# Kernel tuning notes

Measured on AMD Instinct MI355X. Metric: run time of the kernel, lower is better.

Reference implementation:

```python
import jax, jax.numpy as jnp
import numpy as np

N, D, H = 1024, 256, 512


def _linear_init(key, fan_in, fan_out):
    kw, kb = jax.random.split(key)
    bound = 1.0 / np.sqrt(fan_in)
    w = jax.random.uniform(kw, (fan_in, fan_out), jnp.float32, -bound, bound)
    b = jax.random.uniform(kb, (fan_out,), jnp.float32, -bound, bound)
    return w, b


def setup_inputs() -> dict:
    key = jax.random.key(0)
    ks = jax.random.split(key, 8)
    domain_a = jax.random.normal(ks[0], (N, D), jnp.float32)
    domain_b = jax.random.normal(ks[1], (N, D), jnp.float32)
    mu_w0, mu_b0 = _linear_init(ks[2], D, H)
    mu_w1, mu_b1 = _linear_init(ks[3], H, H)
    mu_w2, mu_b2 = _linear_init(ks[4], H, D)
    lv_w0, lv_b0 = _linear_init(ks[5], D, H)
    lv_w1, lv_b1 = _linear_init(ks[6], H, H)
    lv_w2, lv_b2 = _linear_init(ks[7], H, D)
    return dict(domain_a=domain_a, domain_b=domain_b,
                mu_w0=mu_w0, mu_b0=mu_b0, mu_w1=mu_w1, mu_b1=mu_b1, mu_w2=mu_w2, mu_b2=mu_b2,
                lv_w0=lv_w0, lv_b0=lv_b0, lv_w1=lv_w1, lv_b1=lv_b1, lv_w2=lv_w2, lv_b2=lv_b2)


def _net(x, ws, bs, final_act):
    h = x
    for i in range(len(ws)):
        h = h @ ws[i] + bs[i]
        if i < len(ws) - 1:
            h = jax.nn.relu(h)
    return final_act(h)


def _l2norm(h):
    # L2NormEncoder == F.normalize(dim=-1), eps clamp like torch
    n = jnp.maximum(jnp.linalg.norm(h, axis=-1, keepdims=True), 1e-12)
    return h / n


def reference(domain_a, domain_b, mu_w0, mu_b0, mu_w1, mu_b1, mu_w2, mu_b2,
              lv_w0, lv_b0, lv_w1, lv_b1, lv_w2, lv_b2):
    mu_ws, mu_bs = [mu_w0, mu_w1, mu_w2], [mu_b0, mu_b1, mu_b2]
    lv_ws, lv_bs = [lv_w0, lv_w1, lv_w2], [lv_b0, lv_b1, lv_b2]

    # ---- embedding-model loss: prob-model params frozen (requires_grad=False) ----
    sg = jax.lax.stop_gradient
    mu = _net(domain_a, [sg(w) for w in mu_ws], [sg(b) for b in mu_bs], _l2norm)
    log_var = _net(domain_a, [sg(w) for w in lv_ws], [sg(b) for b in lv_bs], jnp.tanh)
    inv_var = jnp.exp(-log_var)                                  # [N, D]
    pos_probs = jnp.sum(-(domain_b - mu) ** 2 * inv_var - log_var, axis=-1)  # [N]
    # pairwise: [i, j, d] = b[j, d] - mu[i, d]; mean over j
    diff2_mean = jnp.mean((domain_b[None, :, :] - mu[:, None, :]) ** 2, axis=1)  # [N, D]
    neg_probs = jnp.sum(-diff2_mean * inv_var - log_var, axis=-1)  # [N]
    embed_model_loss = jnp.mean(pos_probs - neg_probs)

    # ---- prob-model loss: embeddings detached, params trainable ----
    a_d, b_d = sg(domain_a), sg(domain_b)
    mu2 = _net(a_d, mu_ws, mu_bs, _l2norm)
    lv2 = _net(a_d, lv_ws, lv_bs, jnp.tanh)
    prob_model_loss = jnp.mean(jnp.sum((b_d - mu2) ** 2 * jnp.exp(-lv2) + lv2, axis=-1))

    emb_coef, prob_coef = 1.0, 1.0
    loss = emb_coef * embed_model_loss + prob_coef * prob_model_loss
    return loss
```

## Files before the change

### kernel.cpp

```cpp
#include <hip/hip_runtime.h>
#include <hip/hip_fp16.h>

#define N_ROWS 1024
#define DIM 256
#define HID 512

typedef _Float16 half_t;
typedef __attribute__((ext_vector_type(8))) _Float16 half8v;
typedef __attribute__((ext_vector_type(16))) float f32x16;

#define WS_CH 2560
#define AS_CH 2560

struct Params {
    const float* a;
    const float* b;
    const float* w[6];
    const float* bias[6];
    unsigned* c1;
    unsigned* c2;
    unsigned* c3;
    unsigned* cs;
    float* acc;
    unsigned* done;
    float* part_s;
    float* part_s2;
    float* raw[2];
    half_t* h1[2];
    half_t* h2[2];
    float* out;
};

__device__ __forceinline__ void flag_add(unsigned* c) {
    asm volatile("s_waitcnt vmcnt(0)" ::: "memory");
    __syncthreads();
    if (threadIdx.x == 0)
        __hip_atomic_fetch_add(c, 1u, __ATOMIC_RELAXED, __HIP_MEMORY_SCOPE_AGENT);
}
__device__ __forceinline__ void flag_wait(unsigned* c, unsigned tgt) {
    if (threadIdx.x == 0) {
        while (__hip_atomic_load(c, __ATOMIC_RELAXED, __HIP_MEMORY_SCOPE_AGENT) < tgt)
            __builtin_amdgcn_s_sleep(1);
        asm volatile("" ::: "memory");
    }
    __syncthreads();
}

template <int K>
__device__ __forceinline__ void stage_W(const float* __restrict__ W, const int Nout,
                                        const int bn, half_t* __restrict__ Ws) {
    const int tid = threadIdx.x;
    const int wk0 = tid >> 4, wn0 = (tid & 15) * 4;
    #pragma unroll 2
    for (int c = 0; c < K / 32; ++c) {
        float4 v0 = *(const float4*)&W[(c * 32 + wk0) * Nout + bn + wn0];
        float4 v1 = *(const float4*)&W[(c * 32 + wk0 + 16) * Nout + bn + wn0];
        half_t* dst = Ws + c * WS_CH;
        #pragma unroll
        for (int s = 0; s < 2; ++s) {
            const int wk = wk0 + s * 16;
            float4 v = s ? v1 : v0;
            #pragma unroll
            for (int j = 0; j < 4; ++j) {
                const int row = wn0 + j;
                const int cidx = (((wk >> 3) ^ ((row >> 3) & 3)) * 8) + (wk & 7);
                float e = (j == 0) ? v.x : (j == 1) ? v.y : (j == 2) ? v.z : v.w;
                dst[row * 40 + cidx] = (half_t)e;
            }
        }
    }
}

template <int K, int AF32, int MODE>
__device__ __forceinline__ void gemm_phase(const void* __restrict__ Av,
                                           const float* __restrict__ bias,
                                           void* __restrict__ Cp,
                                           const int Nout, const int bm, const int bn,
                                           const half_t* __restrict__ Ws,
                                           half_t* __restrict__ As) {
    const int tid = threadIdx.x;
    const int wave = tid >> 6, lane = tid & 63;
    const int wr = (wave >> 1) * 32, wc = (wave & 1) * 32;
    const int lr = lane & 31, hi = lane >> 5;
    const int sr = tid >> 2, skb = tid & 3;
    const int adst = (skb ^ ((sr >> 3) & 3)) * 8;
    const int ra = wr + lr, rb = wc + lr;
    const int sa = (ra >> 3) & 3, sb = (rb >> 3) & 3;
    const int a0off = (hi ^ sa) * 8, a1off = ((hi + 2) ^ sa) * 8;
    const int b0off = (hi ^ sb) * 8, b1off = ((hi + 2) ^ sb) * 8;
    constexpr int NC = K >> 5;

    const float* Af = (const float*)Av;
    const half_t* Ah = (const half_t*)Av;

    f32x16 acc;
    #pragma unroll
    for (int i = 0; i < 16; ++i) acc[i] = 0.f;

    float4 r0a, r0b, r1a, r1b;
    #define LOAD_A(c, xa, xb)                                                   \
        do {                                                                    \
            if (AF32) {                                                         \
                xa = *(const float4*)&Af[(bm + sr) * K + (c) * 32 + skb * 8];   \
                xb = *(const float4*)&Af[(bm + sr) * K + (c) * 32 + skb * 8 + 4]; \
            } else {                                                            \
                xa = *(const float4*)&Ah[(bm + sr) * K + (c) * 32 + skb * 8];   \
            }                                                                   \
        } while (0)
    #define WRITE_A(buf, xa, xb)                                                \
        do {                                                                    \
            half_t* d = As + (buf) * AS_CH + sr * 40 + adst;                    \
            if (AF32) {                                                         \
                half8v h;                                                       \
                h[0] = (half_t)xa.x; h[1] = (half_t)xa.y;                       \
                h[2] = (half_t)xa.z; h[3] = (half_t)xa.w;                       \
                h[4] = (half_t)xb.x; h[5] = (half_t)xb.y;                       \
                h[6] = (half_t)xb.z; h[7] = (half_t)xb.w;                       \
                *(half8v*)d = h;                                                \
            } else {                                                            \
                *(float4*)d = xa;                                               \
            }                                                                   \
        } while (0)

    LOAD_A(0, r0a, r0b);
    LOAD_A(1, r1a, r1b);
    WRITE_A(0, r0a, r0b);
    if (NC > 2) LOAD_A(2, r0a, r0b);

    for (int c = 0; c < NC; ++c) {
        const int w = c + 1;
        if (w < NC) {
            if (w & 1) { WRITE_A(w % 3, r1a, r1b); }
            else       { WRITE_A(w % 3, r0a, r0b); }
        }
        const int fch = c + 3;
        if (fch < NC) {
            if (fch & 1) { LOAD_A(fch, r1a, r1b); }
            else         { LOAD_A(fch, r0a, r0b); }
        }
        __syncthreads();
        const half_t* ab = As + (c % 3) * AS_CH;
        const half_t* wb = Ws + c * WS_CH;
        half8v av0 = *(const half8v*)&ab[ra * 40 + a0off];
        half8v bv0 = *(const half8v*)&wb[rb * 40 + b0off];
        acc = __builtin_amdgcn_mfma_f32_32x32x16_f16(av0, bv0, acc, 0, 0, 0);
        half8v av1 = *(const half8v*)&ab[ra * 40 + a1off];
        half8v bv1 = *(const half8v*)&wb[rb * 40 + b1off];
        acc = __builtin_amdgcn_mfma_f32_32x32x16_f16(av1, bv1, acc, 0, 0, 0);
    }
    #undef LOAD_A
    #undef WRITE_A

    const int col = bn + wc + lr;
    const float bv = bias[col];
    const int rbase = bm + wr + 4 * hi;
    #pragma unroll
    for (int r = 0; r < 16; ++r) {
        const int row = rbase + (r & 3) + 8 * (r >> 2);
        float v = acc[r] + bv;
        if (MODE == 0) {
            v = fmaxf(v, 0.f);
            union { half_t h; unsigned short u; } cv;
            cv.h = (half_t)v;
            __hip_atomic_store((unsigned short*)Cp + row * Nout + col, cv.u,
                               __ATOMIC_RELAXED, __HIP_MEMORY_SCOPE_AGENT);
        } else {
            __hip_atomic_store((float*)Cp + row * Nout + col, v,
                               __ATOMIC_RELAXED, __HIP_MEMORY_SCOPE_AGENT);
        }
    }
}

__global__ void __launch_bounds__(256) fused_kernel(Params p) {
    __shared__ alignas(16) char smem[98304];
    half_t* Ws = (half_t*)smem;
    half_t* As = (half_t*)(smem + 81920);

    const int bid = blockIdx.x, tid = threadIdx.x;
    const int net = bid & 1;
    const int m = (bid >> 1) & 15;
    const int n = bid >> 5;
    const int bm = m * 64;

    stage_W<DIM>(p.w[net], HID, n * 64, Ws);
    __syncthreads();
    gemm_phase<DIM, 1, 0>(p.a, p.bias[net], p.h1[net], HID, bm, n * 64, Ws, As);
    flag_add(&p.c1[net * 16 + m]);

    if (net == 1 && n >= 4) {
        const int idx = m * 4 + (n - 4);
        const int r0 = idx * 16, d = tid;
        float s = 0.f, s2 = 0.f;
        #pragma unroll
        for (int r = 0; r < 16; ++r) {
            float v = p.b[(r0 + r) * DIM + d];
            s += v; s2 = fmaf(v, v, s2);
        }
        __hip_atomic_store(&p.part_s[idx * DIM + d], s, __ATOMIC_RELAXED,
                           __HIP_MEMORY_SCOPE_AGENT);
        __hip_atomic_store(&p.part_s2[idx * DIM + d], s2, __ATOMIC_RELAXED,
                           __HIP_MEMORY_SCOPE_AGENT);
        flag_add(p.cs);
    }

    stage_W<HID>(p.w[2 + net], HID, n * 64, Ws);
    flag_wait(&p.c1[net * 16 + m], 8);
    gemm_phase<HID, 0, 0>(p.h1[net], p.bias[2 + net], p.h2[net], HID, bm, n * 64, Ws, As);
    flag_add(&p.c2[net * 16 + m]);

    if (n < 4) {
        stage_W<HID>(p.w[4 + net], DIM, n * 64, Ws);
        flag_wait(&p.c2[net * 16 + m], 8);
        gemm_phase<HID, 0, 1>(p.h2[net], p.bias[4 + net], p.raw[net], DIM, bm, n * 64, Ws, As);
        flag_add(&p.c3[m]);
    }

    if (net == 0 && n >= 4) {
        const int q = n - 4;
        flag_wait(p.cs, 64);
        flag_wait(&p.c3[m], 8);

        float* ebL  = (float*)smem;
        float* eb2L = ebL + 256;
        float* bsum = ebL + 512;
        {
            const int d = tid;
            float s = 0.f, s2 = 0.f;
            #pragma unroll 8
            for (int j = 0; j < 64; ++j) {
                s  += p.part_s[j * DIM + d];
                s2 += p.part_s2[j * DIM + d];
            }
            ebL[d]  = s  * (1.f / (float)N_ROWS);
            eb2L[d] = s2 * (1.f / (float)N_ROWS);
        }
        if (tid == 0) *bsum = 0.f;
        __syncthreads();

        const float* mu_raw = p.raw[0];
        const float* lv_raw = p.raw[1];
        const int wave = tid >> 6, lane = tid & 63;
        const int rbase = m * 64 + q * 16;
        float wacc = 0.f;
        #pragma unroll
        for (int rr = 0; rr < 4; ++rr) {
            const int i = rbase + wave * 4 + rr;
            float m4[4], l4[4], ss = 0.f;
            #pragma unroll
            for (int t = 0; t < 4; ++t) {
                const int d = lane + t * 64;
                m4[t] = mu_raw[i * DIM + d];
                l4[t] = lv_raw[i * DIM + d];
                ss = fmaf(m4[t], m4[t], ss);
            }
            #pragma unroll
            for (int o = 32; o > 0; o >>= 1) ss += __shfl_xor(ss, o, 64);
            const float inv_norm = 1.f / fmaxf(sqrtf(ss), 1e-12f);
            #pragma unroll
            for (int t = 0; t < 4; ++t) {
                const int d = lane + t * 64;
                float mu = m4[t] * inv_norm;
                float lv = tanhf(l4[t]);
                float iv = expf(-lv);
                float diff2 = fmaf(mu, mu, fmaf(-2.f * mu, ebL[d], eb2L[d]));
                wacc += fmaf(diff2, iv, lv);
            }
        }
        #pragma unroll
        for (int o = 32; o > 0; o >>= 1) wacc += __shfl_xor(wacc, o, 64);
        if (lane == 0) atomicAdd(bsum, wacc);
        __syncthreads();
        if (tid == 0) {
            atomicAdd(p.acc, *bsum);
            asm volatile("s_waitcnt vmcnt(0)" ::: "memory");
            unsigned prev = __hip_atomic_fetch_add(p.done, 1u, __ATOMIC_RELAXED,
                                                   __HIP_MEMORY_SCOPE_AGENT);
            if (prev == 63u) {
                float v = __hip_atomic_load(p.acc, __ATOMIC_RELAXED, __HIP_MEMORY_SCOPE_AGENT);
                p.out[0] = v * (1.0f / (float)N_ROWS);
            }
        }
    }
}

extern "C" void kernel_launch(void* const* d_in, const int* in_sizes, int n_in,
                              void* d_out, int out_size, void* d_ws, size_t ws_size,
                              hipStream_t stream) {
    Params p;
    p.a = (const float*)d_in[0];
    p.b = (const float*)d_in[1];
    p.w[0] = (const float*)d_in[2];  p.bias[0] = (const float*)d_in[3];
    p.w[2] = (const float*)d_in[4];  p.bias[2] = (const float*)d_in[5];
    p.w[4] = (const float*)d_in[6];  p.bias[4] = (const float*)d_in[7];
    p.w[1] = (const float*)d_in[8];  p.bias[1] = (const float*)d_in[9];
    p.w[3] = (const float*)d_in[10]; p.bias[3] = (const float*)d_in[11];
    p.w[5] = (const float*)d_in[12]; p.bias[5] = (const float*)d_in[13];

    float* f = (float*)d_ws;
    p.c1   = (unsigned*)f;
    p.c2   = (unsigned*)(f + 32);
    p.c3   = (unsigned*)(f + 64);
    p.cs   = (unsigned*)(f + 80);
    p.acc  = f + 81;
    p.done = (unsigned*)(f + 82);
    p.part_s  = f + 128;
    p.part_s2 = p.part_s + 64 * DIM;
    p.raw[0]  = p.part_s2 + 64 * DIM;
    p.raw[1]  = p.raw[0] + N_ROWS * DIM;
    half_t* hb = (half_t*)(p.raw[1] + N_ROWS * DIM);
    p.h1[0] = hb;  hb += N_ROWS * HID;
    p.h1[1] = hb;  hb += N_ROWS * HID;
    p.h2[0] = hb;  hb += N_ROWS * HID;
    p.h2[1] = hb;  hb += N_ROWS * HID;
    p.out = (float*)d_out;

    hipMemsetAsync(d_ws, 0, 512, stream);
    fused_kernel<<<256, 256, 0, stream>>>(p);
}
```

Measured before the change: 37.24 us.

## Load GEMM A operands directly into registers and pad sync counters apart

The A operand of each GEMM phase is now loaded straight from global memory into registers in MFMA fragment layout, prefetched several chunks ahead. This replaces the shared-memory A staging buffer and removes the per-chunk __syncthreads. Weight fragments are also prefetched from LDS into registers four chunks ahead, and the loop is fully unrolled. Sync counters are spaced 16 words apart so each sits on its own cache line, which needs a larger memset. The costs are much higher register pressure from the prefetch arrays, and each wave reading its A rows uncoalesced and redundantly from global memory.

```diff
diff --git a/kernel.cpp b/kernel.cpp
--- a/kernel.cpp
+++ b/kernel.cpp
@@ -4,13 +4,13 @@
 #define N_ROWS 1024
 #define DIM 256
 #define HID 512
+#define CTR 16
 
 typedef _Float16 half_t;
 typedef __attribute__((ext_vector_type(8))) _Float16 half8v;
 typedef __attribute__((ext_vector_type(16))) float f32x16;
 
 #define WS_CH 2560
-#define AS_CH 2560
 
 struct Params {
     const float* a;
@@ -41,9 +41,9 @@
     if (threadIdx.x == 0) {
         while (__hip_atomic_load(c, __ATOMIC_RELAXED, __HIP_MEMORY_SCOPE_AGENT) < tgt)
             __builtin_amdgcn_s_sleep(1);
-        asm volatile("" ::: "memory");
     }
     __syncthreads();
+    asm volatile("" ::: "memory");
 }
 
 template <int K>
@@ -76,80 +76,75 @@
                                            const float* __restrict__ bias,
                                            void* __restrict__ Cp,
                                            const int Nout, const int bm, const int bn,
-                                           const half_t* __restrict__ Ws,
-                                           half_t* __restrict__ As) {
+                                           const half_t* __restrict__ Ws) {
     const int tid = threadIdx.x;
     const int wave = tid >> 6, lane = tid & 63;
     const int wr = (wave >> 1) * 32, wc = (wave & 1) * 32;
     const int lr = lane & 31, hi = lane >> 5;
-    const int sr = tid >> 2, skb = tid & 3;
-    const int adst = (skb ^ ((sr >> 3) & 3)) * 8;
-    const int ra = wr + lr, rb = wc + lr;
-    const int sa = (ra >> 3) & 3, sb = (rb >> 3) & 3;
-    const int a0off = (hi ^ sa) * 8, a1off = ((hi + 2) ^ sa) * 8;
+    const int rb = wc + lr;
+    const int sb = (rb >> 3) & 3;
     const int b0off = (hi ^ sb) * 8, b1off = ((hi + 2) ^ sb) * 8;
+    const int wrow = rb * 40;
     constexpr int NC = K >> 5;
-
-    const float* Af = (const float*)Av;
-    const half_t* Ah = (const half_t*)Av;
+    constexpr int PFA = AF32 ? 4 : 8;
+
+    const float*  Af = (const float*)Av + (bm + wr + lr) * K;
+    const half_t* Ah = (const half_t*)Av + (bm + wr + lr) * K;
 
     f32x16 acc;
     #pragma unroll
     for (int i = 0; i < 16; ++i) acc[i] = 0.f;
 
-    float4 r0a, r0b, r1a, r1b;
-    #define LOAD_A(c, xa, xb)                                                   \
-        do {                                                                    \
-            if (AF32) {                                                         \
-                xa = *(const float4*)&Af[(bm + sr) * K + (c) * 32 + skb * 8];   \
-                xb = *(const float4*)&Af[(bm + sr) * K + (c) * 32 + skb * 8 + 4]; \
-            } else {                                                            \
-                xa = *(const float4*)&Ah[(bm + sr) * K + (c) * 32 + skb * 8];   \
-            }                                                                   \
+    half8v ah[8][2];
+    float4 af[4][4];
+    half8v wb[4][2];
+
+    #define ISSUE_A(c)                                                            \
+        do {                                                                      \
+            if (AF32) {                                                           \
+                af[(c) & 3][0] = *(const float4*)&Af[(c) * 32 + hi * 8];          \
+                af[(c) & 3][1] = *(const float4*)&Af[(c) * 32 + hi * 8 + 4];      \
+                af[(c) & 3][2] = *(const float4*)&Af[(c) * 32 + 16 + hi * 8];     \
+                af[(c) & 3][3] = *(const float4*)&Af[(c) * 32 + 16 + hi * 8 + 4]; \
+            } else {                                                              \
+                ah[(c) & 7][0] = *(const half8v*)&Ah[(c) * 32 + hi * 8];          \
+                ah[(c) & 7][1] = *(const half8v*)&Ah[(c) * 32 + 16 + hi * 8];     \
+            }                                                                     \
         } while (0)
-    #define WRITE_A(buf, xa, xb)                                                \
-        do {                                                                    \
-            half_t* d = As + (buf) * AS_CH + sr * 40 + adst;                    \
-            if (AF32) {                                                         \
-                half8v h;                                                       \
-                h[0] = (half_t)xa.x; h[1] = (half_t)xa.y;                       \
-                h[2] = (half_t)xa.z; h[3] = (half_t)xa.w;                       \
-                h[4] = (half_t)xb.x; h[5] = (half_t)xb.y;                       \
-                h[6] = (half_t)xb.z; h[7] = (half_t)xb.w;                       \
-                *(half8v*)d = h;                                                \
-            } else {                                                            \
-                *(float4*)d = xa;                                               \
-            }                                                                   \
+    #define ISSUE_W(c)                                                            \
+        do {                                                                      \
+            const half_t* wp_ = Ws + (c) * WS_CH + wrow;                          \
+            wb[(c) & 3][0] = *(const half8v*)&wp_[b0off];                         \
+            wb[(c) & 3][1] = *(const half8v*)&wp_[b1off];                         \
         } while (0)
 
-    LOAD_A(0, r0a, r0b);
-    LOAD_A(1, r1a, r1b);
-    WRITE_A(0, r0a, r0b);
-    if (NC > 2) LOAD_A(2, r0a, r0b);
-
+    #pragma unroll
+    for (int c = 0; c < PFA; ++c) ISSUE_A(c);
+    #pragma unroll
+    for (int c = 0; c < 4; ++c) ISSUE_W(c);
+
+    #pragma unroll
     for (int c = 0; c < NC; ++c) {
-        const int w = c + 1;
-        if (w < NC) {
-            if (w & 1) { WRITE_A(w % 3, r1a, r1b); }
-            else       { WRITE_A(w % 3, r0a, r0b); }
-        }
-        const int fch = c + 3;
-        if (fch < NC) {
-            if (fch & 1) { LOAD_A(fch, r1a, r1b); }
-            else         { LOAD_A(fch, r0a, r0b); }
-        }
-        __syncthreads();
-        const half_t* ab = As + (c % 3) * AS_CH;
-        const half_t* wb = Ws + c * WS_CH;
-        half8v av0 = *(const half8v*)&ab[ra * 40 + a0off];
-        half8v bv0 = *(const half8v*)&wb[rb * 40 + b0off];
+        half8v av0, av1;
+        if (AF32) {
+            float4 x0 = af[c & 3][0], x1 = af[c & 3][1];
+            float4 x2 = af[c & 3][2], x3 = af[c & 3][3];
+            av0[0] = (half_t)x0.x; av0[1] = (half_t)x0.y; av0[2] = (half_t)x0.z; av0[3] = (half_t)x0.w;
+            av0[4] = (half_t)x1.x; av0[5] = (half_t)x1.y; av0[6] = (half_t)x1.z; av0[7] = (half_t)x1.w;
+            av1[0] = (half_t)x2.x; av1[1] = (half_t)x2.y; av1[2] = (half_t)x2.z; av1[3] = (half_t)x2.w;
+            av1[4] = (half_t)x3.x; av1[5] = (half_t)x3.y; av1[6] = (half_t)x3.z; av1[7] = (half_t)x3.w;
+        } else {
+            av0 = ah[c & 7][0];
+            av1 = ah[c & 7][1];
+        }
+        if (c + PFA < NC) ISSUE_A(c + PFA);
+        half8v bv0 = wb[c & 3][0], bv1 = wb[c & 3][1];
+        if (c + 4 < NC) ISSUE_W(c + 4);
         acc = __builtin_amdgcn_mfma_f32_32x32x16_f16(av0, bv0, acc, 0, 0, 0);
-        half8v av1 = *(const half8v*)&ab[ra * 40 + a1off];
-        half8v bv1 = *(const half8v*)&wb[rb * 40 + b1off];
         acc = __builtin_amdgcn_mfma_f32_32x32x16_f16(av1, bv1, acc, 0, 0, 0);
     }
-    #undef LOAD_A
-    #undef WRITE_A
+    #undef ISSUE_A
+    #undef ISSUE_W
 
     const int col = bn + wc + lr;
     const float bv = bias[col];
@@ -172,9 +167,8 @@
 }
 
 __global__ void __launch_bounds__(256) fused_kernel(Params p) {
-    __shared__ alignas(16) char smem[98304];
+    __shared__ alignas(16) char smem[81920];
     half_t* Ws = (half_t*)smem;
-    half_t* As = (half_t*)(smem + 81920);
 
     const int bid = blockIdx.x, tid = threadIdx.x;
     const int net = bid & 1;
@@ -184,8 +178,8 @@
 
     stage_W<DIM>(p.w[net], HID, n * 64, Ws);
     __syncthreads();
-    gemm_phase<DIM, 1, 0>(p.a, p.bias[net], p.h1[net], HID, bm, n * 64, Ws, As);
-    flag_add(&p.c1[net * 16 + m]);
+    gemm_phase<DIM, 1, 0>(p.a, p.bias[net], p.h1[net], HID, bm, n * 64, Ws);
+    flag_add(p.c1 + (net * 16 + m) * CTR);
 
     if (net == 1 && n >= 4) {
         const int idx = m * 4 + (n - 4);
@@ -204,21 +198,21 @@
     }
 
     stage_W<HID>(p.w[2 + net], HID, n * 64, Ws);
-    flag_wait(&p.c1[net * 16 + m], 8);
-    gemm_phase<HID, 0, 0>(p.h1[net], p.bias[2 + net], p.h2[net], HID, bm, n * 64, Ws, As);
-    flag_add(&p.c2[net * 16 + m]);
+    flag_wait(p.c1 + (net * 16 + m) * CTR, 8);
+    gemm_phase<HID, 0, 0>(p.h1[net], p.bias[2 + net], p.h2[net], HID, bm, n * 64, Ws);
+    flag_add(p.c2 + (net * 16 + m) * CTR);
 
     if (n < 4) {
         stage_W<HID>(p.w[4 + net], DIM, n * 64, Ws);
-        flag_wait(&p.c2[net * 16 + m], 8);
-        gemm_phase<HID, 0, 1>(p.h2[net], p.bias[4 + net], p.raw[net], DIM, bm, n * 64, Ws, As);
-        flag_add(&p.c3[m]);
+        flag_wait(p.c2 + (net * 16 + m) * CTR, 8);
+        gemm_phase<HID, 0, 1>(p.h2[net], p.bias[4 + net], p.raw[net], DIM, bm, n * 64, Ws);
+        flag_add(p.c3 + m * CTR);
     }
 
     if (net == 0 && n >= 4) {
         const int q = n - 4;
         flag_wait(p.cs, 64);
-        flag_wait(&p.c3[m], 8);
+        flag_wait(p.c3 + m * CTR, 8);
 
         float* ebL  = (float*)smem;
         float* eb2L = ebL + 256;
@@ -298,12 +292,12 @@
 
     float* f = (float*)d_ws;
     p.c1   = (unsigned*)f;
-    p.c2   = (unsigned*)(f + 32);
-    p.c3   = (unsigned*)(f + 64);
-    p.cs   = (unsigned*)(f + 80);
-    p.acc  = f + 81;
-    p.done = (unsigned*)(f + 82);
-    p.part_s  = f + 128;
+    p.c2   = (unsigned*)(f + 512);
+    p.c3   = (unsigned*)(f + 1024);
+    p.cs   = (unsigned*)(f + 1280);
+    p.acc  = f + 1296;
+    p.done = (unsigned*)(f + 1312);
+    p.part_s  = f + 2048;
     p.part_s2 = p.part_s + 64 * DIM;
     p.raw[0]  = p.part_s2 + 64 * DIM;
     p.raw[1]  = p.raw[0] + N_ROWS * DIM;
@@ -314,6 +308,6 @@
     p.h2[1] = hb;  hb += N_ROWS * HID;
     p.out = (float*)d_out;
 
-    hipMemsetAsync(d_ws, 0, 512, stream);
+    hipMemsetAsync(d_ws, 0, 6144, stream);
     fused_kernel<<<256, 256, 0, stream>>>(p);
 }
```

Result: slower. 38.20 us (+2.6%).
